# Kernel optimization log

Hardware: AMD Instinct MI355X
Metric: run time of the kernel (lower is better)

## Reference

```python
import jax, jax.numpy as jnp
import numpy as np

N_HEADS = 4
D_HEAD = 32  # out_features // n_heads = 128 // 4
NEG_SLOPE = 0.2


def setup_inputs() -> dict:
    key = jax.random.key(0)
    k_x, k_adj, k_w, k_a = jax.random.split(key, 4)
    B, N, F_in, F_out = 4, 2048, 128, 128
    x = jax.random.normal(k_x, (B, N, F_in), dtype=jnp.float32)
    adj = jax.random.randint(k_adj, (B, N, N), 0, 2, dtype=jnp.int32)
    # Linear weight stored as [in, out] (torch stores [out, in]; math identical: x @ W)
    w_scale = np.sqrt(2.0 / (F_in + F_out))  # xavier-ish
    W = jax.random.normal(k_w, (F_in, F_out), dtype=jnp.float32) * w_scale
    a = jax.random.normal(k_a, (N_HEADS, 2 * D_HEAD), dtype=jnp.float32) * np.sqrt(2.0 / (2 * D_HEAD))
    return {"x": x, "adj": adj, "W": W, "a": a}


def reference(x, adj, W, a):
    B, N, _ = x.shape
    # project and split heads: [B, H, N, D]
    h = jnp.einsum('bnf,fo->bno', x, W).reshape(B, N, N_HEADS, D_HEAD).transpose(0, 2, 1, 3)
    # additive attention logits
    e_src = jnp.einsum('bhnd,hd->bhn', h, a[:, :D_HEAD])  # [B,H,N]
    e_dst = jnp.einsum('bhnd,hd->bhn', h, a[:, D_HEAD:])  # [B,H,N]
    e = e_src[:, :, :, None] + e_dst[:, :, None, :]       # [B,H,N,N]
    e = jnp.where(e > 0, e, NEG_SLOPE * e)                # leaky_relu(0.2)
    mask = (adj[:, None, :, :] == 0)                      # [B,1,N,N] -> broadcast over heads
    e = jnp.where(mask, -jnp.inf, e)
    alpha = jax.nn.softmax(e, axis=-1)                    # dropout omitted (eval mode)
    out = jnp.einsum('bhnm,bhmd->bhnd', alpha, h)         # weighted aggregation
    out = out.transpose(0, 2, 1, 3).reshape(B, N, N_HEADS * D_HEAD)
    return jax.nn.elu(out)
```

## Files before the change

### kernel.cpp

```cpp
#include <hip/hip_runtime.h>
#include <hip/hip_bf16.h>

#define BB 4
#define NN 2048
#define FIN 128
#define NH 4
#define DH 32
#define NS 0.2f

typedef unsigned int u32;
typedef unsigned short u16;
typedef unsigned long long u64;
typedef __attribute__((ext_vector_type(8))) short short8;
typedef __attribute__((ext_vector_type(4))) float f32x4;
typedef __attribute__((ext_vector_type(4))) unsigned int u32x4;

#define OFF_ES   0
#define OFF_PQ   32768
#define OFF_HT   65536
#define OFF_BITS 589824

__device__ __forceinline__ u16 f2bf_rne(float f) {
  unsigned u = __float_as_uint(f);
  return (u16)((u + 0x7fffu + ((u >> 16) & 1u)) >> 16);
}

__device__ __forceinline__ int bitmask(u32 w, int e) {
#if __has_builtin(__builtin_amdgcn_sbfe)
  return __builtin_amdgcn_sbfe((int)w, e, 1);
#else
  return ((int)(w << (31 - e))) >> 31;
#endif
}

template<int N> __device__ __forceinline__ void vmwait() {
  asm volatile("s_waitcnt vmcnt(%0)" :: "n"(N) : "memory");
  __builtin_amdgcn_sched_barrier(0);
}
__device__ __forceinline__ u32x4 gld4(const void* p) {
  u32x4 r;
  asm volatile("global_load_dwordx4 %0, %1, off" : "=v"(r) : "v"(p));
  return r;
}
__device__ __forceinline__ u32 gld1(const void* p) {
  u32 r;
  asm volatile("global_load_dword %0, %1, off" : "=v"(r) : "v"(p));
  return r;
}

__global__ __launch_bounds__(256) void k_pack(const int* __restrict__ adj,
                                              u32* __restrict__ bitsT) {
  __shared__ u32 tile[64][4];
  const int row0 = blockIdx.x * 4;
  const int wv = threadIdx.x >> 6;
  const int lane = threadIdx.x & 63;
  const int b = row0 >> 11, n0 = row0 & (NN - 1);
  const int* src = adj + (size_t)(row0 + wv) * NN;
#pragma unroll 8
  for (int it = 0; it < 32; ++it) {
    const u64 m = __ballot(src[it * 64 + lane] != 0);
    if (lane == 0) {
      tile[2 * it][wv] = (u32)m;
      tile[2 * it + 1][wv] = (u32)(m >> 32);
    }
  }
  __syncthreads();
  const int word = threadIdx.x >> 2, r = threadIdx.x & 3;
  bitsT[(size_t)b * 64 * NN + (size_t)word * NN + n0 + r] = tile[word][r];
}

__global__ __launch_bounds__(256) void k_proj(
    const float* __restrict__ x, const float* __restrict__ W,
    const float* __restrict__ a, u16* __restrict__ hT,
    float* __restrict__ e_src, u32* __restrict__ PQ) {
  __shared__ float Ws[FIN * 128];
  const int tid = threadIdx.x;
  const int f = tid & 127, g = tid >> 7;
  const float4* Wg4 = (const float4*)W;
  float4* Ws4 = (float4*)Ws;
#pragma unroll
  for (int t = 0; t < 16; ++t) Ws4[t * 256 + tid] = Wg4[t * 256 + tid];
  __syncthreads();

  const int rb = blockIdx.x * 16 + g * 8;
  const int head = f >> 5, d = f & 31;
  const int b = rb >> 11, n0 = rb & (NN - 1);
  const int bh = b * NH + head;
  const float a_s = a[head * (2 * DH) + d];
  const float a_d = a[head * (2 * DH) + DH + d];

  float acc[8];
#pragma unroll
  for (int r = 0; r < 8; ++r) acc[r] = 0.f;

  const float* xb = x + (size_t)rb * FIN;
  for (int k = 0; k < FIN; ++k) {
    const float wv = Ws[k * 128 + f];
#pragma unroll
    for (int r = 0; r < 8; ++r) acc[r] = fmaf(wv, xb[r * FIN + k], acc[r]);
  }

  u16 hs[8];
#pragma unroll
  for (int r = 0; r < 8; ++r) hs[r] = f2bf_rne(acc[r]);
  u16* dst = hT + ((size_t)bh * DH + d) * NN + n0;
  *(int4*)dst = *(int4*)&hs[0];

#pragma unroll
  for (int r = 0; r < 8; ++r) {
    float s1 = acc[r] * a_s;
    float s2 = acc[r] * a_d;
#pragma unroll
    for (int off = 16; off >= 1; off >>= 1) {
      s1 += __shfl_xor(s1, off);
      s2 += __shfl_xor(s2, off);
    }
    if (d == 0) {
      e_src[(size_t)bh * NN + n0 + r] = s1;
      const u32 pb = f2bf_rne(__expf(s2));
      const u32 qb = f2bf_rne(__expf(NS * s2));
      PQ[(size_t)bh * NN + n0 + r] = (qb << 16) | pb;
    }
  }
}

__global__ __launch_bounds__(256, 2) void k_attn(
    const u16* __restrict__ hT, const float* __restrict__ e_src,
    const u32* __restrict__ PQv, const u32* __restrict__ bitsT,
    float* __restrict__ out) {
  __shared__ float part[4][64][33];
  __shared__ float sp[4][4][16];

  const int bid = blockIdx.x;
  const int bh = bid >> 5;
  const int it = bid & 31;
  const int b = bh >> 2, head = bh & 3;

  const int w = threadIdx.x >> 6;
  const int lane = threadIdx.x & 63;
  const int lg = lane >> 4, lm = lane & 15;

  float A[4], B[4];
#pragma unroll
  for (int rs = 0; rs < 4; ++rs) {
    const float es = e_src[(size_t)bh * NN + it * 64 + rs * 16 + lm];
    A[rs] = __expf(es);
    B[rs] = __expf(NS * es);
  }

  const int jwbase = w * 512;
  const u32* PQb = PQv + (size_t)bh * NN + jwbase;
  const u16* hb0 = hT + ((size_t)bh * DH + lm) * NN + jwbase;
  const u16* hb1 = hT + ((size_t)bh * DH + 16 + lm) * NN + jwbase;
  const u32* btb = bitsT + (size_t)b * 64 * NN + (size_t)(w * 16) * NN + it * 64 + lm;
  const int shamt = lg * 8;
  const int jb = lg * 8;

  short8 ones;
#pragma unroll
  for (int e = 0; e < 8; ++e) ones[e] = (short)0x3F80;

  f32x4 acc00 = {0,0,0,0}, acc01 = {0,0,0,0};
  f32x4 acc10 = {0,0,0,0}, acc11 = {0,0,0,0};
  f32x4 acc20 = {0,0,0,0}, acc21 = {0,0,0,0};
  f32x4 acc30 = {0,0,0,0}, acc31 = {0,0,0,0};
  f32x4 accS0 = {0,0,0,0}, accS1 = {0,0,0,0};
  f32x4 accS2 = {0,0,0,0}, accS3 = {0,0,0,0};

  u32x4 pqa_[4], pqb_[4], h0_[4], h1_[4];
  u32 b0_[4], b1_[4], b2_[4], b3_[4];

#define ISSUE(tt, s) do { \
    const int jjI = (tt) * 32 + jb; \
    h0_[s]  = gld4(hb0 + jjI); \
    h1_[s]  = gld4(hb1 + jjI); \
    pqa_[s] = gld4(PQb + jjI); \
    pqb_[s] = gld4(PQb + jjI + 4); \
    const u32* bw_ = btb + (size_t)(tt) * NN; \
    b0_[s] = gld1(bw_); \
    b1_[s] = gld1(bw_ + 16); \
    b2_[s] = gld1(bw_ + 32); \
    b3_[s] = gld1(bw_ + 48); \
  } while (0)

#define COMPUTE(s) do { \
    const u32x4 pqa = pqa_[s]; \
    const u32x4 pqb = pqb_[s]; \
    const short8 hv0 = __builtin_bit_cast(short8, h0_[s]); \
    const short8 hv1 = __builtin_bit_cast(short8, h1_[s]); \
    const u32 wsh0 = b0_[s] >> shamt; \
    const u32 wsh1 = b1_[s] >> shamt; \
    const u32 wsh2 = b2_[s] >> shamt; \
    const u32 wsh3 = b3_[s] >> shamt; \
    short8 af0, af1, af2, af3; \
    _Pragma("unroll") \
    for (int e = 0; e < 8; ++e) { \
      const u32 pq = (e < 4) ? pqa[e] : pqb[e - 4]; \
      const float Pf = __uint_as_float(pq << 16); \
      const float Qf = __uint_as_float(pq & 0xffff0000u); \
      float w0 = fmaxf(A[0] * Pf, B[0] * Qf); \
      float w1 = fmaxf(A[1] * Pf, B[1] * Qf); \
      float w2 = fmaxf(A[2] * Pf, B[2] * Qf); \
      float w3 = fmaxf(A[3] * Pf, B[3] * Qf); \
      w0 = __int_as_float(__float_as_int(w0) & bitmask(wsh0, e)); \
      w1 = __int_as_float(__float_as_int(w1) & bitmask(wsh1, e)); \
      w2 = __int_as_float(__float_as_int(w2) & bitmask(wsh2, e)); \
      w3 = __int_as_float(__float_as_int(w3) & bitmask(wsh3, e)); \
      af0[e] = (short)__builtin_bit_cast(unsigned short, __float2bfloat16(w0)); \
      af1[e] = (short)__builtin_bit_cast(unsigned short, __float2bfloat16(w1)); \
      af2[e] = (short)__builtin_bit_cast(unsigned short, __float2bfloat16(w2)); \
      af3[e] = (short)__builtin_bit_cast(unsigned short, __float2bfloat16(w3)); \
    } \
    acc00 = __builtin_amdgcn_mfma_f32_16x16x32_bf16(af0, hv0, acc00, 0, 0, 0); \
    acc01 = __builtin_amdgcn_mfma_f32_16x16x32_bf16(af0, hv1, acc01, 0, 0, 0); \
    acc10 = __builtin_amdgcn_mfma_f32_16x16x32_bf16(af1, hv0, acc10, 0, 0, 0); \
    acc11 = __builtin_amdgcn_mfma_f32_16x16x32_bf16(af1, hv1, acc11, 0, 0, 0); \
    acc20 = __builtin_amdgcn_mfma_f32_16x16x32_bf16(af2, hv0, acc20, 0, 0, 0); \
    acc21 = __builtin_amdgcn_mfma_f32_16x16x32_bf16(af2, hv1, acc21, 0, 0, 0); \
    acc30 = __builtin_amdgcn_mfma_f32_16x16x32_bf16(af3, hv0, acc30, 0, 0, 0); \
    acc31 = __builtin_amdgcn_mfma_f32_16x16x32_bf16(af3, hv1, acc31, 0, 0, 0); \
    accS0 = __builtin_amdgcn_mfma_f32_16x16x32_bf16(af0, ones, accS0, 0, 0, 0); \
    accS1 = __builtin_amdgcn_mfma_f32_16x16x32_bf16(af1, ones, accS1, 0, 0, 0); \
    accS2 = __builtin_amdgcn_mfma_f32_16x16x32_bf16(af2, ones, accS2, 0, 0, 0); \
    accS3 = __builtin_amdgcn_mfma_f32_16x16x32_bf16(af3, ones, accS3, 0, 0, 0); \
  } while (0)

  vmwait<0>();
  ISSUE(0, 0);
  ISSUE(1, 1);
  ISSUE(2, 2);
#pragma unroll
  for (int t = 0; t < 13; ++t) {
    ISSUE(t + 3, (t + 3) & 3);
    vmwait<24>();
    COMPUTE(t & 3);
  }
  vmwait<16>(); COMPUTE(1);
  vmwait<8>();  COMPUTE(2);
  vmwait<0>();  COMPUTE(3);

#undef ISSUE
#undef COMPUTE

#pragma unroll
  for (int r = 0; r < 4; ++r) {
    const int rl = lg * 4 + r;
    part[w][rl][lm]           = acc00[r];
    part[w][rl][16 + lm]      = acc01[r];
    part[w][16 + rl][lm]      = acc10[r];
    part[w][16 + rl][16 + lm] = acc11[r];
    part[w][32 + rl][lm]      = acc20[r];
    part[w][32 + rl][16 + lm] = acc21[r];
    part[w][48 + rl][lm]      = acc30[r];
    part[w][48 + rl][16 + lm] = acc31[r];
  }
  if (lm == 0) {
#pragma unroll
    for (int r = 0; r < 4; ++r) {
      sp[w][0][lg * 4 + r] = accS0[r];
      sp[w][1][lg * 4 + r] = accS1[r];
      sp[w][2][lg * 4 + r] = accS2[r];
      sp[w][3][lg * 4 + r] = accS3[r];
    }
  }
  __syncthreads();

  const int tid = threadIdx.x;
#pragma unroll
  for (int t = 0; t < 8; ++t) {
    const int idx = t * 256 + tid;
    const int row = idx >> 5, d = idx & 31;
    const float v = part[0][row][d] + part[1][row][d] +
                    part[2][row][d] + part[3][row][d];
    const float s = sp[0][row >> 4][row & 15] + sp[1][row >> 4][row & 15] +
                    sp[2][row >> 4][row & 15] + sp[3][row >> 4][row & 15];
    const float o = v / s;
    const int n = it * 64 + row;
    out[((size_t)b * NN + n) * 128 + head * 32 + d] =
        o > 0.f ? o : (__expf(o) - 1.f);
  }
}

extern "C" void kernel_launch(void* const* d_in, const int* in_sizes, int n_in,
                              void* d_out, int out_size, void* d_ws, size_t ws_size,
                              hipStream_t stream) {
  const float* x = (const float*)d_in[0];
  const int* adj = (const int*)d_in[1];
  const float* W = (const float*)d_in[2];
  const float* a = (const float*)d_in[3];
  float* out = (float*)d_out;
  float* ws = (float*)d_ws;

  float* e_src = ws + OFF_ES;
  u32* PQv = (u32*)(ws + OFF_PQ);
  u16* hT = (u16*)(ws + OFF_HT);
  u32* bitsT = (u32*)(ws + OFF_BITS);

  k_pack<<<(BB * NN) / 4, 256, 0, stream>>>(adj, bitsT);
  k_proj<<<(BB * NN) / 16, 256, 0, stream>>>(x, W, a, hT, e_src, PQv);
  k_attn<<<BB * NH * 32, 256, 0, stream>>>(hT, e_src, PQv, bitsT, out);
}
```

Before: 60.10 us.

## Stage h tiles into LDS via global_load_lds with XOR swizzle, triple buffering

Replaces direct per-lane global loads of the bf16 h operand with global-to-LDS direct loads into a swizzled per-wave shared buffer, then reads MFMA B fragments from LDS. The pipeline moves from 4-deep 32-column stages to 3-deep 64-column stages, and the epilogue reuses the same shared buffer for partial sums after a barrier. The aim is more coalesced 16-byte global accesses and lower VGPR pressure for in-flight h data. In exchange it adds LDS traffic and relies on vmcnt covering LDS-direct loads with no explicit LDS wait, which is a correctness risk.

```diff
diff --git a/kernel.cpp b/kernel.cpp
--- a/kernel.cpp
+++ b/kernel.cpp
@@ -46,6 +46,11 @@
   u32 r;
   asm volatile("global_load_dword %0, %1, off" : "=v"(r) : "v"(p));
   return r;
+}
+__device__ __forceinline__ void gload_lds16(const u16* g, u16* l) {
+  __builtin_amdgcn_global_load_lds(
+      (const __attribute__((address_space(1))) u32*)g,
+      (__attribute__((address_space(3))) u32*)l, 16, 0, 0);
 }
 
 __global__ __launch_bounds__(256) void k_pack(const int* __restrict__ adj,
@@ -128,8 +133,7 @@
     const u16* __restrict__ hT, const float* __restrict__ e_src,
     const u32* __restrict__ PQv, const u32* __restrict__ bitsT,
     float* __restrict__ out) {
-  __shared__ float part[4][64][33];
-  __shared__ float sp[4][4][16];
+  __shared__ __align__(16) u16 smem[4][3][2048];
 
   const int bid = blockIdx.x;
   const int bh = bid >> 5;
@@ -150,11 +154,14 @@
 
   const int jwbase = w * 512;
   const u32* PQb = PQv + (size_t)bh * NN + jwbase;
-  const u16* hb0 = hT + ((size_t)bh * DH + lm) * NN + jwbase;
-  const u16* hb1 = hT + ((size_t)bh * DH + 16 + lm) * NN + jwbase;
   const u32* btb = bitsT + (size_t)b * 64 * NN + (size_t)(w * 16) * NN + it * 64 + lm;
   const int shamt = lg * 8;
   const int jb = lg * 8;
+
+  const int sd = lane >> 3;
+  const int sjq = lane & 7;
+  const u16* gsrc0 = hT + (size_t)bh * DH * NN + jwbase
+                   + (size_t)sd * NN + ((sjq ^ sd) * 8);
 
   short8 ones;
 #pragma unroll
@@ -167,80 +174,93 @@
   f32x4 accS0 = {0,0,0,0}, accS1 = {0,0,0,0};
   f32x4 accS2 = {0,0,0,0}, accS3 = {0,0,0,0};
 
-  u32x4 pqa_[4], pqb_[4], h0_[4], h1_[4];
-  u32 b0_[4], b1_[4], b2_[4], b3_[4];
-
-#define ISSUE(tt, s) do { \
-    const int jjI = (tt) * 32 + jb; \
-    h0_[s]  = gld4(hb0 + jjI); \
-    h1_[s]  = gld4(hb1 + jjI); \
-    pqa_[s] = gld4(PQb + jjI); \
-    pqb_[s] = gld4(PQb + jjI + 4); \
-    const u32* bw_ = btb + (size_t)(tt) * NN; \
-    b0_[s] = gld1(bw_); \
-    b1_[s] = gld1(bw_ + 16); \
-    b2_[s] = gld1(bw_ + 32); \
-    b3_[s] = gld1(bw_ + 48); \
+  u32x4 pqa_[3][2], pqb_[3][2];
+  u32 b0_[3][2], b1_[3][2], b2_[3][2], b3_[3][2];
+
+#define ISSUE(ss, bf) do { \
+    const u16* g_ = gsrc0 + (ss) * 64; \
+    u16* l_ = &smem[w][bf][0]; \
+    gload_lds16(g_ + 0 * 8 * NN, l_ + 0 * 512); \
+    gload_lds16(g_ + 1 * 8 * NN, l_ + 1 * 512); \
+    gload_lds16(g_ + 2 * 8 * NN, l_ + 2 * 512); \
+    gload_lds16(g_ + 3 * 8 * NN, l_ + 3 * 512); \
+    pqa_[bf][0] = gld4(PQb + (ss) * 64 + jb); \
+    pqb_[bf][0] = gld4(PQb + (ss) * 64 + jb + 4); \
+    pqa_[bf][1] = gld4(PQb + (ss) * 64 + 32 + jb); \
+    pqb_[bf][1] = gld4(PQb + (ss) * 64 + 32 + jb + 4); \
+    const u32* bw0_ = btb + (size_t)((ss) * 2) * NN; \
+    const u32* bw1_ = btb + (size_t)((ss) * 2 + 1) * NN; \
+    b0_[bf][0] = gld1(bw0_);      b1_[bf][0] = gld1(bw0_ + 16); \
+    b2_[bf][0] = gld1(bw0_ + 32); b3_[bf][0] = gld1(bw0_ + 48); \
+    b0_[bf][1] = gld1(bw1_);      b1_[bf][1] = gld1(bw1_ + 16); \
+    b2_[bf][1] = gld1(bw1_ + 32); b3_[bf][1] = gld1(bw1_ + 48); \
   } while (0)
 
-#define COMPUTE(s) do { \
-    const u32x4 pqa = pqa_[s]; \
-    const u32x4 pqb = pqb_[s]; \
-    const short8 hv0 = __builtin_bit_cast(short8, h0_[s]); \
-    const short8 hv1 = __builtin_bit_cast(short8, h1_[s]); \
-    const u32 wsh0 = b0_[s] >> shamt; \
-    const u32 wsh1 = b1_[s] >> shamt; \
-    const u32 wsh2 = b2_[s] >> shamt; \
-    const u32 wsh3 = b3_[s] >> shamt; \
-    short8 af0, af1, af2, af3; \
+#define COMPUTE(bf) do { \
+    const u16* lb_ = &smem[w][bf][0]; \
     _Pragma("unroll") \
-    for (int e = 0; e < 8; ++e) { \
-      const u32 pq = (e < 4) ? pqa[e] : pqb[e - 4]; \
-      const float Pf = __uint_as_float(pq << 16); \
-      const float Qf = __uint_as_float(pq & 0xffff0000u); \
-      float w0 = fmaxf(A[0] * Pf, B[0] * Qf); \
-      float w1 = fmaxf(A[1] * Pf, B[1] * Qf); \
-      float w2 = fmaxf(A[2] * Pf, B[2] * Qf); \
-      float w3 = fmaxf(A[3] * Pf, B[3] * Qf); \
-      w0 = __int_as_float(__float_as_int(w0) & bitmask(wsh0, e)); \
-      w1 = __int_as_float(__float_as_int(w1) & bitmask(wsh1, e)); \
-      w2 = __int_as_float(__float_as_int(w2) & bitmask(wsh2, e)); \
-      w3 = __int_as_float(__float_as_int(w3) & bitmask(wsh3, e)); \
-      af0[e] = (short)__builtin_bit_cast(unsigned short, __float2bfloat16(w0)); \
-      af1[e] = (short)__builtin_bit_cast(unsigned short, __float2bfloat16(w1)); \
-      af2[e] = (short)__builtin_bit_cast(unsigned short, __float2bfloat16(w2)); \
-      af3[e] = (short)__builtin_bit_cast(unsigned short, __float2bfloat16(w3)); \
+    for (int c = 0; c < 2; ++c) { \
+      const int blk = ((c * 4 + lg) ^ (lm & 7)) * 8; \
+      const short8 hv0 = *(const short8*)(lb_ + lm * 64 + blk); \
+      const short8 hv1 = *(const short8*)(lb_ + (16 + lm) * 64 + blk); \
+      const u32x4 pqa = pqa_[bf][c]; \
+      const u32x4 pqb = pqb_[bf][c]; \
+      const u32 wsh0 = b0_[bf][c] >> shamt; \
+      const u32 wsh1 = b1_[bf][c] >> shamt; \
+      const u32 wsh2 = b2_[bf][c] >> shamt; \
+      const u32 wsh3 = b3_[bf][c] >> shamt; \
+      short8 af0, af1, af2, af3; \
+      _Pragma("unroll") \
+      for (int e = 0; e < 8; ++e) { \
+        const u32 pq = (e < 4) ? pqa[e] : pqb[e - 4]; \
+        const float Pf = __uint_as_float(pq << 16); \
+        const float Qf = __uint_as_float(pq & 0xffff0000u); \
+        float w0 = fmaxf(A[0] * Pf, B[0] * Qf); \
+        float w1 = fmaxf(A[1] * Pf, B[1] * Qf); \
+        float w2 = fmaxf(A[2] * Pf, B[2] * Qf); \
+        float w3 = fmaxf(A[3] * Pf, B[3] * Qf); \
+        w0 = __int_as_float(__float_as_int(w0) & bitmask(wsh0, e)); \
+        w1 = __int_as_float(__float_as_int(w1) & bitmask(wsh1, e)); \
+        w2 = __int_as_float(__float_as_int(w2) & bitmask(wsh2, e)); \
+        w3 = __int_as_float(__float_as_int(w3) & bitmask(wsh3, e)); \
+        af0[e] = (short)__builtin_bit_cast(unsigned short, __float2bfloat16(w0)); \
+        af1[e] = (short)__builtin_bit_cast(unsigned short, __float2bfloat16(w1)); \
+        af2[e] = (short)__builtin_bit_cast(unsigned short, __float2bfloat16(w2)); \
+        af3[e] = (short)__builtin_bit_cast(unsigned short, __float2bfloat16(w3)); \
+      } \
+      acc00 = __builtin_amdgcn_mfma_f32_16x16x32_bf16(af0, hv0, acc00, 0, 0, 0); \
+      acc01 = __builtin_amdgcn_mfma_f32_16x16x32_bf16(af0, hv1, acc01, 0, 0, 0); \
+      acc10 = __builtin_amdgcn_mfma_f32_16x16x32_bf16(af1, hv0, acc10, 0, 0, 0); \
+      acc11 = __builtin_amdgcn_mfma_f32_16x16x32_bf16(af1, hv1, acc11, 0, 0, 0); \
+      acc20 = __builtin_amdgcn_mfma_f32_16x16x32_bf16(af2, hv0, acc20, 0, 0, 0); \
+      acc21 = __builtin_amdgcn_mfma_f32_16x16x32_bf16(af2, hv1, acc21, 0, 0, 0); \
+      acc30 = __builtin_amdgcn_mfma_f32_16x16x32_bf16(af3, hv0, acc30, 0, 0, 0); \
+      acc31 = __builtin_amdgcn_mfma_f32_16x16x32_bf16(af3, hv1, acc31, 0, 0, 0); \
+      accS0 = __builtin_amdgcn_mfma_f32_16x16x32_bf16(af0, ones, accS0, 0, 0, 0); \
+      accS1 = __builtin_amdgcn_mfma_f32_16x16x32_bf16(af1, ones, accS1, 0, 0, 0); \
+      accS2 = __builtin_amdgcn_mfma_f32_16x16x32_bf16(af2, ones, accS2, 0, 0, 0); \
+      accS3 = __builtin_amdgcn_mfma_f32_16x16x32_bf16(af3, ones, accS3, 0, 0, 0); \
     } \
-    acc00 = __builtin_amdgcn_mfma_f32_16x16x32_bf16(af0, hv0, acc00, 0, 0, 0); \
-    acc01 = __builtin_amdgcn_mfma_f32_16x16x32_bf16(af0, hv1, acc01, 0, 0, 0); \
-    acc10 = __builtin_amdgcn_mfma_f32_16x16x32_bf16(af1, hv0, acc10, 0, 0, 0); \
-    acc11 = __builtin_amdgcn_mfma_f32_16x16x32_bf16(af1, hv1, acc11, 0, 0, 0); \
-    acc20 = __builtin_amdgcn_mfma_f32_16x16x32_bf16(af2, hv0, acc20, 0, 0, 0); \
-    acc21 = __builtin_amdgcn_mfma_f32_16x16x32_bf16(af2, hv1, acc21, 0, 0, 0); \
-    acc30 = __builtin_amdgcn_mfma_f32_16x16x32_bf16(af3, hv0, acc30, 0, 0, 0); \
-    acc31 = __builtin_amdgcn_mfma_f32_16x16x32_bf16(af3, hv1, acc31, 0, 0, 0); \
-    accS0 = __builtin_amdgcn_mfma_f32_16x16x32_bf16(af0, ones, accS0, 0, 0, 0); \
-    accS1 = __builtin_amdgcn_mfma_f32_16x16x32_bf16(af1, ones, accS1, 0, 0, 0); \
-    accS2 = __builtin_amdgcn_mfma_f32_16x16x32_bf16(af2, ones, accS2, 0, 0, 0); \
-    accS3 = __builtin_amdgcn_mfma_f32_16x16x32_bf16(af3, ones, accS3, 0, 0, 0); \
   } while (0)
 
   vmwait<0>();
   ISSUE(0, 0);
   ISSUE(1, 1);
-  ISSUE(2, 2);
-#pragma unroll
-  for (int t = 0; t < 13; ++t) {
-    ISSUE(t + 3, (t + 3) & 3);
-    vmwait<24>();
-    COMPUTE(t & 3);
-  }
-  vmwait<16>(); COMPUTE(1);
-  vmwait<8>();  COMPUTE(2);
-  vmwait<0>();  COMPUTE(3);
+#pragma unroll
+  for (int t = 0; t < 6; ++t) {
+    ISSUE(t + 2, (t + 2) % 3);
+    vmwait<32>();
+    COMPUTE(t % 3);
+  }
+  vmwait<16>(); COMPUTE(0);
+  vmwait<0>();  COMPUTE(1);
 
 #undef ISSUE
 #undef COMPUTE
+
+  __syncthreads();
+  float (*part)[64][33] = (float (*)[64][33]) & smem[0][0][0];
+  float (*sp)[4][16] = (float (*)[4][16])((char*)&smem[0][0][0] + 33792);
 
 #pragma unroll
   for (int r = 0; r < 4; ++r) {
```

Result: no change. 60.33 us (+0.4%).
